# Kernel tuning notes

Measured on AMD Instinct MI355X. Metric: run time of the kernel, lower is better.

## Reference

```python
import jax, jax.numpy as jnp
import numpy as np

D = 4                      # corr_disp / max_displacement
K = 2 * D + 1              # window side -> K*K = 81 displacement channels
C = 256                    # in_channels


def shifted_patches(x, d):
    """x: [B,C,H,W] -> [B,C,K*K,H,W]; patch k=(dy*K+dx) is x shifted by
    (dy-d, dx-d) with zero padding (matches Correlation/NaiveAssemble2 indexing)."""
    B, Ch, H, W = x.shape
    xp = jnp.pad(x, ((0, 0), (0, 0), (d, d), (d, d)))
    k = 2 * d + 1
    sl = [xp[:, :, dy:dy + H, dx:dx + W] for dy in range(k) for dx in range(k)]
    return jnp.stack(sl, axis=2)


def conv2d(x, w, b, pad):
    y = jax.lax.conv_general_dilated(
        x, w, window_strides=(1, 1), padding=[(pad, pad), (pad, pad)],
        dimension_numbers=('NCHW', 'OIHW', 'NCHW'))
    return y + b[None, :, None, None]


def setup_inputs() -> dict:
    key = jax.random.key(0)
    ks = jax.random.split(key, 12)
    B, H, W = 2, 64, 64
    std = 0.01
    return {
        'feat':     jax.random.normal(ks[0], (B, C, H, W), jnp.float32),
        'feat_ref': jax.random.normal(ks[1], (B, C, H, W), jnp.float32),
        # ConcatUpdate conv stack: 2C->256 (1x1), 256->16 (3x3), 16->3 (3x3), 3->2 (3x3)
        'w1': jax.random.normal(ks[2], (256, 2 * C, 1, 1), jnp.float32) * std,
        'b1': jnp.zeros((256,), jnp.float32),
        'w2': jax.random.normal(ks[3], (16, 256, 3, 3), jnp.float32) * std,
        'b2': jnp.zeros((16,), jnp.float32),
        'w3': jax.random.normal(ks[4], (3, 16, 3, 3), jnp.float32) * std,
        'b3': jnp.zeros((3,), jnp.float32),
        'w4': jax.random.normal(ks[5], (2, 3, 3, 3), jnp.float32) * std,
        'b4': jnp.array([1.0, 0.0], jnp.float32),  # init_weights: bias[0]=1, bias[1]=0
    }


def reference(feat, feat_ref, w1, b1, w2, b2, w3, b3, w4, b4):
    # Correlation (cost volume over (2D+1)^2 displacements, kernel_size=1)
    patches = shifted_patches(feat_ref, D)                    # [B,C,K2,H,W]
    aff = jnp.einsum('bchw,bckhw->bkhw', feat, patches)       # [B,K2,H,W]
    # sum-normalize over displacement channels (use_softmax_norm=False)
    aff = aff / (jnp.sum(aff, axis=1, keepdims=True) + 1e-7)
    # NaiveAssemble2: windowed weighted gather of feat_ref
    aligned = jnp.einsum('bkhw,bckhw->bchw', aff, patches)    # [B,C,H,W]
    # ConcatUpdate
    cat = jnp.concatenate([feat, aligned], axis=1)            # [B,2C,H,W]
    h = conv2d(cat, w1, b1, 0)
    h = conv2d(h, w2, b2, 1)
    h = conv2d(h, w3, b3, 1)
    logits = conv2d(h, w4, b4, 1)                             # [B,2,H,W]
    score = jax.nn.softmax(logits, axis=1)
    return score[:, 0:1] * feat + score[:, 1:2] * aligned
```

## Files before the change

kernel.cpp:

```cpp
#include <hip/hip_runtime.h>
#include <hip/hip_bf16.h>
#include <math.h>

#define BATCH 2
#define CCH   256
#define HH    64
#define WW    64
#define PIX   (HH*WW)
#define K2    81
#define BP_N  (BATCH*PIX)

__global__ void k_transpose2(const float* __restrict__ feat,
                             const float* __restrict__ feat_ref,
                             float* __restrict__ featT,
                             float* __restrict__ refT) {
    __shared__ float tile[32][33];
    int z  = blockIdx.z;
    int b  = z & 1;
    const float* in  = (z >> 1) ? feat_ref : feat;
    float*       out = (z >> 1) ? refT     : featT;
    int p0 = blockIdx.x * 32;
    int c0 = blockIdx.y * 32;
    int tx = threadIdx.x;
    int ty = threadIdx.y;
    const float* ib = in  + (size_t)b * CCH * PIX;
    float*       ob = out + (size_t)b * CCH * PIX;
    #pragma unroll
    for (int i = 0; i < 4; i++) {
        int c = c0 + ty + i * 8;
        int p = p0 + tx;
        tile[ty + i * 8][tx] = ib[(size_t)c * PIX + p];
    }
    __syncthreads();
    #pragma unroll
    for (int i = 0; i < 4; i++) {
        int p = p0 + ty + i * 8;
        int c = c0 + tx;
        ob[(size_t)p * CCH + c] = tile[tx][ty + i * 8];
    }
}

__global__ void k_wprep(const float* __restrict__ w1, float* __restrict__ w1t,
                        const float* __restrict__ w2, float* __restrict__ w2t) {
    __shared__ float tile[32][33];
    int blk = blockIdx.x;
    int tid = threadIdx.x;
    if (blk < 128) {
        int c0 = (blk & 15) * 32;
        int o0 = (blk >> 4) * 32;
        int tx = tid & 31;
        int ty = tid >> 5;
        #pragma unroll
        for (int i = 0; i < 4; i++)
            tile[ty + i * 8][tx] = w1[(size_t)(o0 + ty + i * 8) * 512 + c0 + tx];
        __syncthreads();
        #pragma unroll
        for (int i = 0; i < 4; i++)
            w1t[(size_t)(c0 + ty + i * 8) * 256 + o0 + tx] = tile[tx][ty + i * 8];
    } else {
        int i = (blk - 128) * 256 + tid;
        if (i < 16 * 256 * 9) {
            int o  = i / 2304;
            int r  = i % 2304;
            int c  = r / 9;
            int kk = r % 9;
            int cg = c >> 2, ci = c & 3;
            w2t[(((kk * 64 + cg) * 16 + o) << 2) + ci] = w2[i];
        }
    }
}

__global__ void k_corr_assemble(const float* __restrict__ featT,
                                const float* __restrict__ refT,
                                float* __restrict__ alignedT) {
    int blk = blockIdx.x;
    int pr  = ((blk & 7) << 9) | (blk >> 3);
    int bp  = pr << 1;
    int b  = bp >> 12;
    int p  = bp & 4095;
    int h  = p >> 6, w = p & 63;
    int tid = threadIdx.x;

    __shared__ float s_aff0[K2];
    __shared__ float s_aff1[K2];
    __shared__ __align__(8) int2 s_u[96];
    __shared__ int   s_hi_a[32];
    __shared__ int   s_hi_b[32];
    __shared__ int   s_cnt0, s_cnt1;
    __shared__ float s_den0, s_den1;
    __shared__ __align__(16) float s_c0[96];
    __shared__ __align__(16) float s_c1[96];
    __shared__ __align__(16) int   s_po[96];

    int hw = tid >> 5;
    int j  = tid & 31;

    const float* fb = featT + ((size_t)bp << 8) + j;
    float f0[8], f1[8];
    #pragma unroll
    for (int t = 0; t < 8; t++) { f0[t] = fb[32 * t]; f1[t] = fb[256 + 32 * t]; }

    if (tid < K2) { s_aff0[tid] = 0.f; s_aff1[tid] = 0.f; }

    if (tid < 128) {
        int u  = tid;
        int uy = u / 10, ux = u - uy * 10;
        int y  = h + uy - 4, x = w + ux - 4;
        bool valid = (u < 90) && ((unsigned)y < 64u) && ((unsigned)x < 64u);
        int poff = ((y << 6) | x) << 10;
        int meta = (ux << 8) | (uy * 9 + ux);
        unsigned long long m = __ballot(valid);
        int lane   = tid & 63;
        int prefix = __popcll(m & ((1ULL << lane) - 1ULL));
        if (tid < 64) {
            if (valid) s_u[prefix] = make_int2(poff, meta);
            if (tid == 0) s_cnt0 = (int)__popcll(m);
        } else {
            if (valid) { s_hi_a[prefix] = poff; s_hi_b[prefix] = meta; }
            if (tid == 64) s_cnt1 = (int)__popcll(m);
        }
    }
    __syncthreads();
    int n0 = s_cnt0, n1 = s_cnt1;
    int nu = n0 + n1;
    if (tid < n1) s_u[n0 + tid] = make_int2(s_hi_a[tid], s_hi_b[tid]);
    __syncthreads();

    const float* rb  = refT + ((size_t)b << 20);
    const char*  rbj = (const char*)rb + 4 * j;

    int ii = 2 * hw;
    bool act = ii < nu;
    int2 U0 = make_int2(0, 0), U1 = make_int2(0, 0);
    bool has1 = false;
    float r0[8], r1[8];
    if (act) {
        U0 = s_u[ii];
        has1 = (ii + 1) < nu;
        U1 = has1 ? s_u[ii + 1] : U0;
        const char* rp0 = rbj + U0.x;
        const char* rp1 = rbj + U1.x;
        #pragma unroll
        for (int t = 0; t < 8; t++) {
            r0[t] = *(const float*)(rp0 + 128 * t);
            r1[t] = *(const float*)(rp1 + 128 * t);
        }
    }
    while (act) {
        float pa0 = 0.f, pb0 = 0.f, pa1 = 0.f, pb1 = 0.f;
        #pragma unroll
        for (int t = 0; t < 8; t++) {
            pa0 = fmaf(f0[t], r0[t], pa0);
            pb0 = fmaf(f1[t], r0[t], pb0);
            pa1 = fmaf(f0[t], r1[t], pa1);
            pb1 = fmaf(f1[t], r1[t], pb1);
        }
        int  m0c = U0.y, m1c = U1.y;
        bool h1c = has1;

        ii += 16;
        bool nact = ii < nu;
        if (nact) {
            U0 = s_u[ii];
            has1 = (ii + 1) < nu;
            U1 = has1 ? s_u[ii + 1] : U0;
            const char* rp0 = rbj + U0.x;
            const char* rp1 = rbj + U1.x;
            #pragma unroll
            for (int t = 0; t < 8; t++) {
                r0[t] = *(const float*)(rp0 + 128 * t);
                r1[t] = *(const float*)(rp1 + 128 * t);
            }
        }

        pa0 = __fadd_rn(pa0, __shfl_xor(pa0, 8));
        pb0 = __fadd_rn(pb0, __shfl_xor(pb0, 8));
        pa1 = __fadd_rn(pa1, __shfl_xor(pa1, 8));
        pb1 = __fadd_rn(pb1, __shfl_xor(pb1, 8));
        pa0 = __fadd_rn(pa0, __shfl_xor(pa0, 16));
        pb0 = __fadd_rn(pb0, __shfl_xor(pb0, 16));
        pa1 = __fadd_rn(pa1, __shfl_xor(pa1, 16));
        pb1 = __fadd_rn(pb1, __shfl_xor(pb1, 16));
        pa0 = __fadd_rn(pa0, __shfl_xor(pa0, 4));
        pb0 = __fadd_rn(pb0, __shfl_xor(pb0, 4));
        pa1 = __fadd_rn(pa1, __shfl_xor(pa1, 4));
        pb1 = __fadd_rn(pb1, __shfl_xor(pb1, 4));
        pa0 = __fadd_rn(pa0, __shfl_xor(pa0, 2));
        pb0 = __fadd_rn(pb0, __shfl_xor(pb0, 2));
        pa1 = __fadd_rn(pa1, __shfl_xor(pa1, 2));
        pb1 = __fadd_rn(pb1, __shfl_xor(pb1, 2));
        pa0 = __fadd_rn(pa0, __shfl_xor(pa0, 1));
        pb0 = __fadd_rn(pb0, __shfl_xor(pb0, 1));
        pa1 = __fadd_rn(pa1, __shfl_xor(pa1, 1));
        pb1 = __fadd_rn(pb1, __shfl_xor(pb1, 1));
        if (j == 0) {
            int k0 = m0c & 255, ux0 = m0c >> 8;
            if (ux0 < 9) s_aff0[k0] = pa0;
            if (ux0 > 0) s_aff1[k0 - 1] = pb0;
            if (h1c) {
                int k1 = m1c & 255, ux1 = m1c >> 8;
                if (ux1 < 9) s_aff0[k1] = pa1;
                if (ux1 > 0) s_aff1[k1 - 1] = pb1;
            }
        }
        act = nact;
    }
    __syncthreads();

    if (tid < 2) {
        const float* sa = tid ? s_aff1 : s_aff0;
        float s = 0.f;
        for (int k = 0; k < K2; k++) s = __fadd_rn(s, sa[k]);
        float d = __fadd_rn(s, 1e-7f);
        if (tid) s_den1 = d; else s_den0 = d;
    }
    __syncthreads();

    if (tid < nu) {
        int2 uu = s_u[tid];
        int k0 = uu.y & 255, ux = uu.y >> 8;
        s_po[tid] = uu.x;
        s_c0[tid] = (ux < 9) ? __fdiv_rn(s_aff0[k0], s_den0) : 0.f;
        s_c1[tid] = (ux > 0) ? __fdiv_rn(s_aff1[k0 - 1], s_den1) : 0.f;
    }
    __syncthreads();

    const char* rbc = (const char*)rb + ((size_t)tid << 2);
    float a0 = 0.f, a1 = 0.f;
    int i = 0;
    for (; i + 8 <= nu; i += 8) {
        float4 cA0 = *(const float4*)&s_c0[i];
        float4 cA1 = *(const float4*)&s_c0[i + 4];
        float4 cB0 = *(const float4*)&s_c1[i];
        float4 cB1 = *(const float4*)&s_c1[i + 4];
        int4   poA = *(const int4*)&s_po[i];
        int4   poB = *(const int4*)&s_po[i + 4];
        float v0 = *(const float*)(rbc + poA.x);
        float v1 = *(const float*)(rbc + poA.y);
        float v2 = *(const float*)(rbc + poA.z);
        float v3 = *(const float*)(rbc + poA.w);
        float v4 = *(const float*)(rbc + poB.x);
        float v5 = *(const float*)(rbc + poB.y);
        float v6 = *(const float*)(rbc + poB.z);
        float v7 = *(const float*)(rbc + poB.w);
        a0 = fmaf(cA0.x, v0, a0);  a1 = fmaf(cB0.x, v0, a1);
        a0 = fmaf(cA0.y, v1, a0);  a1 = fmaf(cB0.y, v1, a1);
        a0 = fmaf(cA0.z, v2, a0);  a1 = fmaf(cB0.z, v2, a1);
        a0 = fmaf(cA0.w, v3, a0);  a1 = fmaf(cB0.w, v3, a1);
        a0 = fmaf(cA1.x, v4, a0);  a1 = fmaf(cB1.x, v4, a1);
        a0 = fmaf(cA1.y, v5, a0);  a1 = fmaf(cB1.y, v5, a1);
        a0 = fmaf(cA1.z, v6, a0);  a1 = fmaf(cB1.z, v6, a1);
        a0 = fmaf(cA1.w, v7, a0);  a1 = fmaf(cB1.w, v7, a1);
    }
    if (i + 4 <= nu) {
        float4 cA = *(const float4*)&s_c0[i];
        float4 cB = *(const float4*)&s_c1[i];
        int4   po = *(const int4*)&s_po[i];
        float v0 = *(const float*)(rbc + po.x);
        float v1 = *(const float*)(rbc + po.y);
        float v2 = *(const float*)(rbc + po.z);
        float v3 = *(const float*)(rbc + po.w);
        a0 = fmaf(cA.x, v0, a0);  a1 = fmaf(cB.x, v0, a1);
        a0 = fmaf(cA.y, v1, a0);  a1 = fmaf(cB.y, v1, a1);
        a0 = fmaf(cA.z, v2, a0);  a1 = fmaf(cB.z, v2, a1);
        a0 = fmaf(cA.w, v3, a0);  a1 = fmaf(cB.w, v3, a1);
        i += 4;
    }
    for (; i < nu; i++) {
        float v = *(const float*)(rbc + s_po[i]);
        a0 = fmaf(s_c0[i], v, a0);
        a1 = fmaf(s_c1[i], v, a1);
    }
    alignedT[((size_t)bp << 8) + tid]       = a0;
    alignedT[((size_t)(bp + 1) << 8) + tid] = a1;
}

__global__ void k_conv1(const float* __restrict__ featT,
                        const float* __restrict__ alignedT,
                        const float* __restrict__ w1t,
                        const float* __restrict__ b1,
                        float* __restrict__ h1) {
    __shared__ float s_a[2][32][68];
    __shared__ float s_b[2][32][68];
    int m0  = blockIdx.x * 64;
    int n0  = blockIdx.y * 64;
    int tid = threadIdx.x;
    int tx  = tid & 15;
    int ty  = tid >> 4;
    int cq  = tid & 7;
    int pxa = tid >> 3;
    int oq  = tid & 15;
    int cc  = tid >> 4;

    float acc[4][4] = {{0.f}};
    float4 ra0, ra1, rb0, rb1;

#define C1_LOAD(kc_) do {                                                     \
        int c0_ = (kc_) * 32;                                                 \
        const float* asrc_ = (c0_ < 256) ? featT : alignedT;                  \
        int coff_ = (c0_ < 256) ? c0_ : c0_ - 256;                            \
        ra0 = *(const float4*)(asrc_ + ((size_t)(m0 + pxa) << 8) + coff_ + (cq << 2));      \
        ra1 = *(const float4*)(asrc_ + ((size_t)(m0 + 32 + pxa) << 8) + coff_ + (cq << 2)); \
        rb0 = *(const float4*)(w1t + (size_t)(c0_ + cc) * 256 + n0 + (oq << 2));            \
        rb1 = *(const float4*)(w1t + (size_t)(c0_ + 16 + cc) * 256 + n0 + (oq << 2));       \
    } while (0)

#define C1_WRITE(bf_) do {                                                    \
        s_a[bf_][cq * 4 + 0][pxa] = ra0.x;                                    \
        s_a[bf_][cq * 4 + 1][pxa] = ra0.y;                                    \
        s_a[bf_][cq * 4 + 2][pxa] = ra0.z;                                    \
        s_a[bf_][cq * 4 + 3][pxa] = ra0.w;                                    \
        s_a[bf_][cq * 4 + 0][32 + pxa] = ra1.x;                               \
        s_a[bf_][cq * 4 + 1][32 + pxa] = ra1.y;                               \
        s_a[bf_][cq * 4 + 2][32 + pxa] = ra1.z;                               \
        s_a[bf_][cq * 4 + 3][32 + pxa] = ra1.w;                               \
        *(float4*)&s_b[bf_][cc][oq << 2] = rb0;                               \
        *(float4*)&s_b[bf_][16 + cc][oq << 2] = rb1;                          \
    } while (0)

    C1_LOAD(0);
    C1_WRITE(0);
    __syncthreads();

    for (int kc = 0; kc < 16; kc++) {
        int cur = kc & 1;
        if (kc < 15) C1_LOAD(kc + 1);

        #pragma unroll 8
        for (int k = 0; k < 32; k++) {
            float4 av = *(const float4*)&s_a[cur][k][ty << 2];
            float4 bv = *(const float4*)&s_b[cur][k][tx << 2];
            acc[0][0] = fmaf(av.x, bv.x, acc[0][0]);
            acc[0][1] = fmaf(av.x, bv.y, acc[0][1]);
            acc[0][2] = fmaf(av.x, bv.z, acc[0][2]);
            acc[0][3] = fmaf(av.x, bv.w, acc[0][3]);
            acc[1][0] = fmaf(av.y, bv.x, acc[1][0]);
            acc[1][1] = fmaf(av.y, bv.y, acc[1][1]);
            acc[1][2] = fmaf(av.y, bv.z, acc[1][2]);
            acc[1][3] = fmaf(av.y, bv.w, acc[1][3]);
            acc[2][0] = fmaf(av.z, bv.x, acc[2][0]);
            acc[2][1] = fmaf(av.z, bv.y, acc[2][1]);
            acc[2][2] = fmaf(av.z, bv.z, acc[2][2]);
            acc[2][3] = fmaf(av.z, bv.w, acc[2][3]);
            acc[3][0] = fmaf(av.w, bv.x, acc[3][0]);
            acc[3][1] = fmaf(av.w, bv.y, acc[3][1]);
            acc[3][2] = fmaf(av.w, bv.z, acc[3][2]);
            acc[3][3] = fmaf(av.w, bv.w, acc[3][3]);
        }

        if (kc < 15) C1_WRITE(cur ^ 1);
        __syncthreads();
    }

    float4 bias = *(const float4*)(b1 + n0 + tx * 4);
    #pragma unroll
    for (int i = 0; i < 4; i++) {
        int px = m0 + ty * 4 + i;
        float4 v;
        v.x = acc[i][0] + bias.x;
        v.y = acc[i][1] + bias.y;
        v.z = acc[i][2] + bias.z;
        v.w = acc[i][3] + bias.w;
        *(float4*)(h1 + ((size_t)px << 8) + n0 + tx * 4) = v;
    }
}

__global__ void k_conv2(const float* __restrict__ h1,
                        const float* __restrict__ w2t,
                        const float* __restrict__ b2,
                        float* __restrict__ h2) {
    __shared__ float s_in[3][18][68];
    int blk = blockIdx.x;
    int b   = blk >> 8;
    int r   = blk & 255;
    int y   = r >> 2;
    int w0  = (r & 3) * 16;
    int tid = threadIdx.x;
    int o   = tid & 15;
    int ps  = (tid >> 4) & 7;

    const float* hb = h1 + ((size_t)b << 20);

    float4 a0 = {0.f, 0.f, 0.f, 0.f};
    float4 a1 = {0.f, 0.f, 0.f, 0.f};

    for (int chunk = 0; chunk < 4; chunk++) {
        int c0 = chunk << 6;
        for (int i = tid; i < 3 * 18 * 16; i += 256) {
            int c4 = i & 15;
            int pi = (i >> 4) % 18;
            int ri = (i >> 4) / 18;
            int yy = y + ri - 1;
            int xx = w0 + pi - 1;
            float4 v = {0.f, 0.f, 0.f, 0.f};
            if ((unsigned)yy < 64u && (unsigned)xx < 64u)
                v = *(const float4*)(hb + ((size_t)((yy << 6) | xx) << 8) + c0 + (c4 << 2));
            *(float4*)&s_in[ri][pi][c4 << 2] = v;
        }
        __syncthreads();

        #pragma unroll
        for (int kk = 0; kk < 9; kk++) {
            int ky = kk / 3, kx = kk - ky * 3;
            const float* wp = w2t + (((size_t)(kk * 64 + (c0 >> 2)) * 16 + o) << 2);
            #pragma unroll 8
            for (int c4 = 0; c4 < 16; c4++) {
                float4 wv = *(const float4*)(wp + (c4 << 6));
                float4 i0 = *(const float4*)&s_in[ky][ps + kx][c4 << 2];
                float4 i1 = *(const float4*)&s_in[ky][ps + 8 + kx][c4 << 2];
                a0.x = fmaf(wv.x, i0.x, a0.x);
                a0.y = fmaf(wv.y, i0.y, a0.y);
                a0.z = fmaf(wv.z, i0.z, a0.z);
                a0.w = fmaf(wv.w, i0.w, a0.w);
                a1.x = fmaf(wv.x, i1.x, a1.x);
                a1.y = fmaf(wv.y, i1.y, a1.y);
                a1.z = fmaf(wv.z, i1.z, a1.z);
                a1.w = fmaf(wv.w, i1.w, a1.w);
            }
        }
        __syncthreads();
    }

    size_t bp0 = ((size_t)b << 12) + (y << 6) + w0;
    h2[(bp0 + ps) * 16 + o]     = ((a0.x + a0.y) + (a0.z + a0.w)) + b2[o];
    h2[(bp0 + ps + 8) * 16 + o] = ((a1.x + a1.y) + (a1.z + a1.w)) + b2[o];
}

__global__ void k_conv3(const float* __restrict__ h2,
                        const float* __restrict__ w3,
                        const float* __restrict__ b3,
                        float* __restrict__ h3) {
    int bp = blockIdx.x * 256 + threadIdx.x;
    if (bp >= BP_N) return;
    int b = bp >> 12;
    int p = bp & 4095;
    int h = p >> 6, w = p & 63;
    const float* hb = h2 + ((size_t)b << 16);

    float a0 = 0.f, a1 = 0.f, a2 = 0.f;
    #pragma unroll
    for (int kk = 0; kk < 9; kk++) {
        int ky = kk / 3, kx = kk - ky * 3;
        int y = h + ky - 1, x = w + kx - 1;
        if ((unsigned)y >= 64u || (unsigned)x >= 64u) continue;
        const float* ip = hb + (size_t)((y << 6) | x) * 16;
        #pragma unroll
        for (int c = 0; c < 16; c++) {
            float v = ip[c];
            int wi = c * 9 + kk;
            a0 = fmaf(w3[wi],       v, a0);
            a1 = fmaf(w3[144 + wi], v, a1);
            a2 = fmaf(w3[288 + wi], v, a2);
        }
    }
    h3[(size_t)bp * 3 + 0] = a0 + b3[0];
    h3[(size_t)bp * 3 + 1] = a1 + b3[1];
    h3[(size_t)bp * 3 + 2] = a2 + b3[2];
}

__global__ void k_score(const float* __restrict__ h3,
                        const float* __restrict__ w4,
                        const float* __restrict__ b4,
                        float2* __restrict__ score) {
    int bp = blockIdx.x * 256 + threadIdx.x;
    if (bp >= BP_N) return;
    int b = bp >> 12;
    int p = bp & 4095;
    int h = p >> 6, w = p & 63;
    const float* hb = h3 + (size_t)b * PIX * 3;

    float l0 = 0.f, l1 = 0.f;
    #pragma unroll
    for (int kk = 0; kk < 9; kk++) {
        int ky = kk / 3, kx = kk - ky * 3;
        int y = h + ky - 1, x = w + kx - 1;
        if ((unsigned)y >= 64u || (unsigned)x >= 64u) continue;
        const float* ip = hb + (size_t)((y << 6) | x) * 3;
        #pragma unroll
        for (int c = 0; c < 3; c++) {
            float v = ip[c];
            int wi = c * 9 + kk;
            l0 = fmaf(w4[wi],      v, l0);
            l1 = fmaf(w4[27 + wi], v, l1);
        }
    }
    l0 += b4[0];
    l1 += b4[1];

    float m  = fmaxf(l0, l1);
    float e0 = expf(l0 - m);
    float e1 = expf(l1 - m);
    float s  = e0 + e1;
    score[bp] = make_float2(e0 / s, e1 / s);
}

__global__ void k_blend(const float* __restrict__ feat,
                        const float* __restrict__ alignedT,
                        const float2* __restrict__ score,
                        float* __restrict__ out) {
    __shared__ float tile[32][33];
    int b  = blockIdx.z;
    int p0 = blockIdx.x * 32;
    int c0 = blockIdx.y * 32;
    int tx = threadIdx.x;
    int ty = threadIdx.y;

    const float* at = alignedT + ((size_t)b << 20);
    #pragma unroll
    for (int i = 0; i < 4; i++) {
        int p = p0 + ty + i * 8;
        tile[ty + i * 8][tx] = at[((size_t)p << 8) + c0 + tx];
    }
    __syncthreads();

    int p = p0 + tx;
    float2 s = score[(b << 12) + p];
    #pragma unroll
    for (int i = 0; i < 4; i++) {
        int c = c0 + ty + i * 8;
        size_t idx = (((size_t)(b * 256 + c)) << 12) + p;
        out[idx] = __fadd_rn(__fmul_rn(s.x, feat[idx]),
                             __fmul_rn(s.y, tile[tx][ty + i * 8]));
    }
}

extern "C" void kernel_launch(void* const* d_in, const int* in_sizes, int n_in,
                              void* d_out, int out_size, void* d_ws, size_t ws_size,
                              hipStream_t stream) {
    const float* feat     = (const float*)d_in[0];
    const float* feat_ref = (const float*)d_in[1];
    const float* w1 = (const float*)d_in[2];
    const float* b1 = (const float*)d_in[3];
    const float* w2 = (const float*)d_in[4];
    const float* b2 = (const float*)d_in[5];
    const float* w3 = (const float*)d_in[6];
    const float* b3 = (const float*)d_in[7];
    const float* w4 = (const float*)d_in[8];
    const float* b4 = (const float*)d_in[9];
    float* out = (float*)d_out;

    const size_t NCP = (size_t)BATCH * CCH * PIX;
    char* wsb = (char*)d_ws;
    float*  featT    = (float*)wsb;   wsb += NCP * 4;
    float*  refT     = (float*)wsb;   wsb += NCP * 4;
    float*  alignedT = (float*)wsb;   wsb += NCP * 4;
    float*  h1       = (float*)wsb;   wsb += NCP * 4;
    float*  h2       = (float*)wsb;   wsb += (size_t)BP_N * 16 * 4;
    float*  h3       = (float*)wsb;   wsb += (size_t)BP_N * 3 * 4;
    float2* sc       = (float2*)wsb;  wsb += (size_t)BP_N * 8;
    float*  w2t      = (float*)wsb;   wsb += (size_t)16 * 256 * 9 * 4;
    float*  w1t      = (float*)wsb;   wsb += (size_t)512 * 256 * 4;

    dim3 tb(32, 8, 1);
    k_transpose2<<<dim3(PIX / 32, CCH / 32, 4), tb, 0, stream>>>(feat, feat_ref, featT, refT);
    k_wprep<<<272, 256, 0, stream>>>(w1, w1t, w2, w2t);

    k_corr_assemble<<<BP_N / 2, 256, 0, stream>>>(featT, refT, alignedT);
    k_conv1<<<dim3(BP_N / 64, 256 / 64, 1), 256, 0, stream>>>(featT, alignedT, w1t, b1, h1);
    k_conv2<<<BP_N / 16, 256, 0, stream>>>(h1, w2t, b2, h2);
    k_conv3<<<BP_N / 256, 256, 0, stream>>>(h2, w3, b3, h3);
    k_score<<<BP_N / 256, 256, 0, stream>>>(h3, w4, b4, sc);
    k_blend<<<dim3(PIX / 32, CCH / 32, BATCH), tb, 0, stream>>>(feat, alignedT, sc, out);
}
```

Baseline: 216.5 us.

## Process four pixels per block in correlation/assemble and merge prep kernels

```diff
diff --git a/kernel.cpp b/kernel.cpp
--- a/kernel.cpp
+++ b/kernel.cpp
@@ -10,46 +10,44 @@
 #define K2    81
 #define BP_N  (BATCH*PIX)
 
-__global__ void k_transpose2(const float* __restrict__ feat,
-                             const float* __restrict__ feat_ref,
-                             float* __restrict__ featT,
-                             float* __restrict__ refT) {
-    __shared__ float tile[32][33];
-    int z  = blockIdx.z;
-    int b  = z & 1;
-    const float* in  = (z >> 1) ? feat_ref : feat;
-    float*       out = (z >> 1) ? refT     : featT;
-    int p0 = blockIdx.x * 32;
-    int c0 = blockIdx.y * 32;
-    int tx = threadIdx.x;
-    int ty = threadIdx.y;
-    const float* ib = in  + (size_t)b * CCH * PIX;
-    float*       ob = out + (size_t)b * CCH * PIX;
-    #pragma unroll
-    for (int i = 0; i < 4; i++) {
-        int c = c0 + ty + i * 8;
-        int p = p0 + tx;
-        tile[ty + i * 8][tx] = ib[(size_t)c * PIX + p];
-    }
-    __syncthreads();
-    #pragma unroll
-    for (int i = 0; i < 4; i++) {
-        int p = p0 + ty + i * 8;
-        int c = c0 + tx;
-        ob[(size_t)p * CCH + c] = tile[tx][ty + i * 8];
-    }
-}
-
-__global__ void k_wprep(const float* __restrict__ w1, float* __restrict__ w1t,
-                        const float* __restrict__ w2, float* __restrict__ w2t) {
+__global__ void k_prep(const float* __restrict__ feat,
+                       const float* __restrict__ feat_ref,
+                       float* __restrict__ featT,
+                       float* __restrict__ refT,
+                       const float* __restrict__ w1, float* __restrict__ w1t,
+                       const float* __restrict__ w2, float* __restrict__ w2t) {
     __shared__ float tile[32][33];
     int blk = blockIdx.x;
-    int tid = threadIdx.x;
-    if (blk < 128) {
-        int c0 = (blk & 15) * 32;
-        int o0 = (blk >> 4) * 32;
-        int tx = tid & 31;
-        int ty = tid >> 5;
+    int tx  = threadIdx.x;
+    int ty  = threadIdx.y;
+    int tid = ty * 32 + tx;
+    if (blk < 4096) {
+        int z   = blk >> 10;
+        int rem = blk & 1023;
+        int c0  = (rem >> 7) * 32;
+        int p0  = (rem & 127) * 32;
+        int b   = z & 1;
+        const float* in  = (z >> 1) ? feat_ref : feat;
+        float*       out = (z >> 1) ? refT     : featT;
+        const float* ib = in  + (size_t)b * CCH * PIX;
+        float*       ob = out + (size_t)b * CCH * PIX;
+        #pragma unroll
+        for (int i = 0; i < 4; i++) {
+            int c = c0 + ty + i * 8;
+            int p = p0 + tx;
+            tile[ty + i * 8][tx] = ib[(size_t)c * PIX + p];
+        }
+        __syncthreads();
+        #pragma unroll
+        for (int i = 0; i < 4; i++) {
+            int p = p0 + ty + i * 8;
+            int c = c0 + tx;
+            ob[(size_t)p * CCH + c] = tile[tx][ty + i * 8];
+        }
+    } else if (blk < 4224) {
+        int wb = blk - 4096;
+        int c0 = (wb & 15) * 32;
+        int o0 = (wb >> 4) * 32;
         #pragma unroll
         for (int i = 0; i < 4; i++)
             tile[ty + i * 8][tx] = w1[(size_t)(o0 + ty + i * 8) * 512 + c0 + tx];
@@ -58,7 +56,7 @@
         for (int i = 0; i < 4; i++)
             w1t[(size_t)(c0 + ty + i * 8) * 256 + o0 + tx] = tile[tx][ty + i * 8];
     } else {
-        int i = (blk - 128) * 256 + tid;
+        int i = (blk - 4224) * 256 + tid;
         if (i < 16 * 256 * 9) {
             int o  = i / 2304;
             int r  = i % 2304;
@@ -74,39 +72,45 @@
                                 const float* __restrict__ refT,
                                 float* __restrict__ alignedT) {
     int blk = blockIdx.x;
-    int pr  = ((blk & 7) << 9) | (blk >> 3);
-    int bp  = pr << 1;
+    int qd  = ((blk & 7) << 8) | (blk >> 3);
+    int bp  = qd << 2;
     int b  = bp >> 12;
     int p  = bp & 4095;
     int h  = p >> 6, w = p & 63;
     int tid = threadIdx.x;
 
-    __shared__ float s_aff0[K2];
-    __shared__ float s_aff1[K2];
-    __shared__ __align__(8) int2 s_u[96];
-    __shared__ int   s_hi_a[32];
-    __shared__ int   s_hi_b[32];
+    __shared__ float s_aff[4][K2];
+    __shared__ __align__(8) int2 s_u[112];
+    __shared__ int   s_hi_a[48];
+    __shared__ int   s_hi_b[48];
     __shared__ int   s_cnt0, s_cnt1;
-    __shared__ float s_den0, s_den1;
-    __shared__ __align__(16) float s_c0[96];
-    __shared__ __align__(16) float s_c1[96];
-    __shared__ __align__(16) int   s_po[96];
+    __shared__ float s_den[4];
+    __shared__ __align__(16) float s_c[4][112];
+    __shared__ __align__(16) int   s_po[112];
 
     int hw = tid >> 5;
     int j  = tid & 31;
 
     const float* fb = featT + ((size_t)bp << 8) + j;
-    float f0[8], f1[8];
+    float f0[8], f1[8], f2[8], f3[8];
     #pragma unroll
-    for (int t = 0; t < 8; t++) { f0[t] = fb[32 * t]; f1[t] = fb[256 + 32 * t]; }
-
-    if (tid < K2) { s_aff0[tid] = 0.f; s_aff1[tid] = 0.f; }
+    for (int t = 0; t < 8; t++) {
+        f0[t] = fb[32 * t];
+        f1[t] = fb[256 + 32 * t];
+        f2[t] = fb[512 + 32 * t];
+        f3[t] = fb[768 + 32 * t];
+    }
+
+    if (tid < K2) {
+        s_aff[0][tid] = 0.f; s_aff[1][tid] = 0.f;
+        s_aff[2][tid] = 0.f; s_aff[3][tid] = 0.f;
+    }
 
     if (tid < 128) {
         int u  = tid;
-        int uy = u / 10, ux = u - uy * 10;
+        int uy = u / 12, ux = u - uy * 12;
         int y  = h + uy - 4, x = w + ux - 4;
-        bool valid = (u < 90) && ((unsigned)y < 64u) && ((unsigned)x < 64u);
+        bool valid = (u < 108) && ((unsigned)y < 64u) && ((unsigned)x < 64u);
         int poff = ((y << 6) | x) << 10;
         int meta = (ux << 8) | (uy * 9 + ux);
         unsigned long long m = __ballot(valid);
@@ -147,13 +151,18 @@
         }
     }
     while (act) {
-        float pa0 = 0.f, pb0 = 0.f, pa1 = 0.f, pb1 = 0.f;
+        float p00 = 0.f, p01 = 0.f, p02 = 0.f, p03 = 0.f;
+        float p10 = 0.f, p11 = 0.f, p12 = 0.f, p13 = 0.f;
         #pragma unroll
         for (int t = 0; t < 8; t++) {
-            pa0 = fmaf(f0[t], r0[t], pa0);
-            pb0 = fmaf(f1[t], r0[t], pb0);
-            pa1 = fmaf(f0[t], r1[t], pa1);
-            pb1 = fmaf(f1[t], r1[t], pb1);
+            p00 = fmaf(f0[t], r0[t], p00);
+            p01 = fmaf(f1[t], r0[t], p01);
+            p02 = fmaf(f2[t], r0[t], p02);
+            p03 = fmaf(f3[t], r0[t], p03);
+            p10 = fmaf(f0[t], r1[t], p10);
+            p11 = fmaf(f1[t], r1[t], p11);
+            p12 = fmaf(f2[t], r1[t], p12);
+            p13 = fmaf(f3[t], r1[t], p13);
         }
         int  m0c = U0.y, m1c = U1.y;
         bool h1c = has1;
@@ -173,106 +182,131 @@
             }
         }
 
-        pa0 = __fadd_rn(pa0, __shfl_xor(pa0, 8));
-        pb0 = __fadd_rn(pb0, __shfl_xor(pb0, 8));
-        pa1 = __fadd_rn(pa1, __shfl_xor(pa1, 8));
-        pb1 = __fadd_rn(pb1, __shfl_xor(pb1, 8));
-        pa0 = __fadd_rn(pa0, __shfl_xor(pa0, 16));
-        pb0 = __fadd_rn(pb0, __shfl_xor(pb0, 16));
-        pa1 = __fadd_rn(pa1, __shfl_xor(pa1, 16));
-        pb1 = __fadd_rn(pb1, __shfl_xor(pb1, 16));
-        pa0 = __fadd_rn(pa0, __shfl_xor(pa0, 4));
-        pb0 = __fadd_rn(pb0, __shfl_xor(pb0, 4));
-        pa1 = __fadd_rn(pa1, __shfl_xor(pa1, 4));
-        pb1 = __fadd_rn(pb1, __shfl_xor(pb1, 4));
-        pa0 = __fadd_rn(pa0, __shfl_xor(pa0, 2));
-        pb0 = __fadd_rn(pb0, __shfl_xor(pb0, 2));
-        pa1 = __fadd_rn(pa1, __shfl_xor(pa1, 2));
-        pb1 = __fadd_rn(pb1, __shfl_xor(pb1, 2));
-        pa0 = __fadd_rn(pa0, __shfl_xor(pa0, 1));
-        pb0 = __fadd_rn(pb0, __shfl_xor(pb0, 1));
-        pa1 = __fadd_rn(pa1, __shfl_xor(pa1, 1));
-        pb1 = __fadd_rn(pb1, __shfl_xor(pb1, 1));
+#define BFLY(MASK)                                        \
+        p00 = __fadd_rn(p00, __shfl_xor(p00, MASK));      \
+        p01 = __fadd_rn(p01, __shfl_xor(p01, MASK));      \
+        p02 = __fadd_rn(p02, __shfl_xor(p02, MASK));      \
+        p03 = __fadd_rn(p03, __shfl_xor(p03, MASK));      \
+        p10 = __fadd_rn(p10, __shfl_xor(p10, MASK));      \
+        p11 = __fadd_rn(p11, __shfl_xor(p11, MASK));      \
+        p12 = __fadd_rn(p12, __shfl_xor(p12, MASK));      \
+        p13 = __fadd_rn(p13, __shfl_xor(p13, MASK));
+        BFLY(8)
+        BFLY(16)
+        BFLY(4)
+        BFLY(2)
+        BFLY(1)
+#undef BFLY
+
         if (j == 0) {
-            int k0 = m0c & 255, ux0 = m0c >> 8;
-            if (ux0 < 9) s_aff0[k0] = pa0;
-            if (ux0 > 0) s_aff1[k0 - 1] = pb0;
+            int base0 = m0c & 255, ux0 = m0c >> 8;
+            if (ux0 <= 8)              s_aff[0][base0]     = p00;
+            if (ux0 >= 1 && ux0 <= 9)  s_aff[1][base0 - 1] = p01;
+            if (ux0 >= 2 && ux0 <= 10) s_aff[2][base0 - 2] = p02;
+            if (ux0 >= 3)              s_aff[3][base0 - 3] = p03;
             if (h1c) {
-                int k1 = m1c & 255, ux1 = m1c >> 8;
-                if (ux1 < 9) s_aff0[k1] = pa1;
-                if (ux1 > 0) s_aff1[k1 - 1] = pb1;
+                int base1 = m1c & 255, ux1 = m1c >> 8;
+                if (ux1 <= 8)              s_aff[0][base1]     = p10;
+                if (ux1 >= 1 && ux1 <= 9)  s_aff[1][base1 - 1] = p11;
+                if (ux1 >= 2 && ux1 <= 10) s_aff[2][base1 - 2] = p12;
+                if (ux1 >= 3)              s_aff[3][base1 - 3] = p13;
             }
         }
         act = nact;
     }
     __syncthreads();
 
-    if (tid < 2) {
-        const float* sa = tid ? s_aff1 : s_aff0;
+    if (tid < 4) {
+        const float* sa = s_aff[tid];
         float s = 0.f;
         for (int k = 0; k < K2; k++) s = __fadd_rn(s, sa[k]);
-        float d = __fadd_rn(s, 1e-7f);
-        if (tid) s_den1 = d; else s_den0 = d;
+        s_den[tid] = __fadd_rn(s, 1e-7f);
     }
     __syncthreads();
 
     if (tid < nu) {
         int2 uu = s_u[tid];
-        int k0 = uu.y & 255, ux = uu.y >> 8;
+        int base = uu.y & 255, ux = uu.y >> 8;
         s_po[tid] = uu.x;
-        s_c0[tid] = (ux < 9) ? __fdiv_rn(s_aff0[k0], s_den0) : 0.f;
-        s_c1[tid] = (ux > 0) ? __fdiv_rn(s_aff1[k0 - 1], s_den1) : 0.f;
+        s_c[0][tid] = (ux <= 8)              ? __fdiv_rn(s_aff[0][base],     s_den[0]) : 0.f;
+        s_c[1][tid] = (ux >= 1 && ux <= 9)   ? __fdiv_rn(s_aff[1][base - 1], s_den[1]) : 0.f;
+        s_c[2][tid] = (ux >= 2 && ux <= 10)  ? __fdiv_rn(s_aff[2][base - 2], s_den[2]) : 0.f;
+        s_c[3][tid] = (ux >= 3)              ? __fdiv_rn(s_aff[3][base - 3], s_den[3]) : 0.f;
     }
     __syncthreads();
 
     const char* rbc = (const char*)rb + ((size_t)tid << 2);
-    float a0 = 0.f, a1 = 0.f;
+    float a0 = 0.f, a1 = 0.f, a2 = 0.f, a3 = 0.f;
+    float vA[8], vB[8];
+
+#define LOADV(V, BASE) do {                                                   \
+        int4 pA_ = *(const int4*)&s_po[BASE];                                 \
+        int4 pB_ = *(const int4*)&s_po[(BASE) + 4];                           \
+        V[0] = *(const float*)(rbc + pA_.x);                                  \
+        V[1] = *(const float*)(rbc + pA_.y);                                  \
+        V[2] = *(const float*)(rbc + pA_.z);                                  \
+        V[3] = *(const float*)(rbc + pA_.w);                                  \
+        V[4] = *(const float*)(rbc + pB_.x);                                  \
+        V[5] = *(const float*)(rbc + pB_.y);                                  \
+        V[6] = *(const float*)(rbc + pB_.z);                                  \
+        V[7] = *(const float*)(rbc + pB_.w);                                  \
+    } while (0)
+
+#define FMA8(V, BASE) do {                                                    \
+        float4 c0a = *(const float4*)&s_c[0][BASE];                           \
+        float4 c0b = *(const float4*)&s_c[0][(BASE) + 4];                     \
+        float4 c1a = *(const float4*)&s_c[1][BASE];                           \
+        float4 c1b = *(const float4*)&s_c[1][(BASE) + 4];                     \
+        float4 c2a = *(const float4*)&s_c[2][BASE];                           \
+        float4 c2b = *(const float4*)&s_c[2][(BASE) + 4];                     \
+        float4 c3a = *(const float4*)&s_c[3][BASE];                           \
+        float4 c3b = *(const float4*)&s_c[3][(BASE) + 4];                     \
+        a0 = fmaf(c0a.x, V[0], a0); a1 = fmaf(c1a.x, V[0], a1);               \
+        a2 = fmaf(c2a.x, V[0], a2); a3 = fmaf(c3a.x, V[0], a3);               \
+        a0 = fmaf(c0a.y, V[1], a0); a1 = fmaf(c1a.y, V[1], a1);               \
+        a2 = fmaf(c2a.y, V[1], a2); a3 = fmaf(c3a.y, V[1], a3);               \
+        a0 = fmaf(c0a.z, V[2], a0); a1 = fmaf(c1a.z, V[2], a1);               \
+        a2 = fmaf(c2a.z, V[2], a2); a3 = fmaf(c3a.z, V[2], a3);               \
+        a0 = fmaf(c0a.w, V[3], a0); a1 = fmaf(c1a.w, V[3], a1);               \
+        a2 = fmaf(c2a.w, V[3], a2); a3 = fmaf(c3a.w, V[3], a3);               \
+        a0 = fmaf(c0b.x, V[4], a0); a1 = fmaf(c1b.x, V[4], a1);               \
+        a2 = fmaf(c2b.x, V[4], a2); a3 = fmaf(c3b.x, V[4], a3);               \
+        a0 = fmaf(c0b.y, V[5], a0); a1 = fmaf(c1b.y, V[5], a1);               \
+        a2 = fmaf(c2b.y, V[5], a2); a3 = fmaf(c3b.y, V[5], a3);               \
+        a0 = fmaf(c0b.z, V[6], a0); a1 = fmaf(c1b.z, V[6], a1);               \
+        a2 = fmaf(c2b.z, V[6], a2); a3 = fmaf(c3b.z, V[6], a3);               \
+        a0 = fmaf(c0b.w, V[7], a0); a1 = fmaf(c1b.w, V[7], a1);               \
+        a2 = fmaf(c2b.w, V[7], a2); a3 = fmaf(c3b.w, V[7], a3);               \
+    } while (0)
+
     int i = 0;
-    for (; i + 8 <= nu; i += 8) {
-        float4 cA0 = *(const float4*)&s_c0[i];
-        float4 cA1 = *(const float4*)&s_c0[i + 4];
-        float4 cB0 = *(const float4*)&s_c1[i];
-        float4 cB1 = *(const float4*)&s_c1[i + 4];
-        int4   poA = *(const int4*)&s_po[i];
-        int4   poB = *(const int4*)&s_po[i + 4];
-        float v0 = *(const float*)(rbc + poA.x);
-        float v1 = *(const float*)(rbc + poA.y);
-        float v2 = *(const float*)(rbc + poA.z);
-        float v3 = *(const float*)(rbc + poA.w);
-        float v4 = *(const float*)(rbc + poB.x);
-        float v5 = *(const float*)(rbc + poB.y);
-        float v6 = *(const float*)(rbc + poB.z);
-        float v7 = *(const float*)(rbc + poB.w);
-        a0 = fmaf(cA0.x, v0, a0);  a1 = fmaf(cB0.x, v0, a1);
-        a0 = fmaf(cA0.y, v1, a0);  a1 = fmaf(cB0.y, v1, a1);
-        a0 = fmaf(cA0.z, v2, a0);  a1 = fmaf(cB0.z, v2, a1);
-        a0 = fmaf(cA0.w, v3, a0);  a1 = fmaf(cB0.w, v3, a1);
-        a0 = fmaf(cA1.x, v4, a0);  a1 = fmaf(cB1.x, v4, a1);
-        a0 = fmaf(cA1.y, v5, a0);  a1 = fmaf(cB1.y, v5, a1);
-        a0 = fmaf(cA1.z, v6, a0);  a1 = fmaf(cB1.z, v6, a1);
-        a0 = fmaf(cA1.w, v7, a0);  a1 = fmaf(cB1.w, v7, a1);
-    }
-    if (i + 4 <= nu) {
-        float4 cA = *(const float4*)&s_c0[i];
-        float4 cB = *(const float4*)&s_c1[i];
-        int4   po = *(const int4*)&s_po[i];
-        float v0 = *(const float*)(rbc + po.x);
-        float v1 = *(const float*)(rbc + po.y);
-        float v2 = *(const float*)(rbc + po.z);
-        float v3 = *(const float*)(rbc + po.w);
-        a0 = fmaf(cA.x, v0, a0);  a1 = fmaf(cB.x, v0, a1);
-        a0 = fmaf(cA.y, v1, a0);  a1 = fmaf(cB.y, v1, a1);
-        a0 = fmaf(cA.z, v2, a0);  a1 = fmaf(cB.z, v2, a1);
-        a0 = fmaf(cA.w, v3, a0);  a1 = fmaf(cB.w, v3, a1);
-        i += 4;
+    if (nu >= 8) {
+        LOADV(vA, 0);
+        for (i = 0; i + 8 <= nu; i += 8) {
+            bool more = (i + 16 <= nu);
+            if (((i >> 3) & 1) == 0) {
+                if (more) LOADV(vB, i + 8);
+                FMA8(vA, i);
+            } else {
+                if (more) LOADV(vA, i + 8);
+                FMA8(vB, i);
+            }
+        }
     }
     for (; i < nu; i++) {
         float v = *(const float*)(rbc + s_po[i]);
-        a0 = fmaf(s_c0[i], v, a0);
-        a1 = fmaf(s_c1[i], v, a1);
-    }
+        a0 = fmaf(s_c[0][i], v, a0);
+        a1 = fmaf(s_c[1][i], v, a1);
+        a2 = fmaf(s_c[2][i], v, a2);
+        a3 = fmaf(s_c[3][i], v, a3);
+    }
+#undef LOADV
+#undef FMA8
+
     alignedT[((size_t)bp << 8) + tid]       = a0;
     alignedT[((size_t)(bp + 1) << 8) + tid] = a1;
+    alignedT[((size_t)(bp + 2) << 8) + tid] = a2;
+    alignedT[((size_t)(bp + 3) << 8) + tid] = a3;
 }
 
 __global__ void k_conv1(const float* __restrict__ featT,
@@ -552,10 +586,9 @@
     float*  w1t      = (float*)wsb;   wsb += (size_t)512 * 256 * 4;
 
     dim3 tb(32, 8, 1);
-    k_transpose2<<<dim3(PIX / 32, CCH / 32, 4), tb, 0, stream>>>(feat, feat_ref, featT, refT);
-    k_wprep<<<272, 256, 0, stream>>>(w1, w1t, w2, w2t);
-
-    k_corr_assemble<<<BP_N / 2, 256, 0, stream>>>(featT, refT, alignedT);
+    k_prep<<<4368, tb, 0, stream>>>(feat, feat_ref, featT, refT, w1, w1t, w2, w2t);
+
+    k_corr_assemble<<<BP_N / 4, 256, 0, stream>>>(featT, refT, alignedT);
     k_conv1<<<dim3(BP_N / 64, 256 / 64, 1), 256, 0, stream>>>(featT, alignedT, w1t, b1, h1);
     k_conv2<<<BP_N / 16, 256, 0, stream>>>(h1, w2t, b2, h2);
     k_conv3<<<BP_N / 256, 256, 0, stream>>>(h2, w3, b3, h3);
```

New measurement: 225.4 us. 1.04x slower.
